# Kernel tuning notes

Measured on AMD Instinct MI355X. Metric: run time of the kernel, lower is better.

The kernel has to match this reference:

```python
import jax, jax.numpy as jnp
import numpy as np
from jax import lax

B, T = 32, 256
VOCAB, WDIM, MDIM = 50000, 300, 50
HID, NLAYERS, NCLASSES = 512, 2, 3


def _init(key, shape, scale):
    return (jax.random.normal(key, shape, dtype=jnp.float32) * scale)


def setup_inputs() -> dict:
    key = jax.random.key(0)
    ks = jax.random.split(key, 20)
    inputs_seq = jax.random.randint(ks[0], (B, T), 0, VOCAB, dtype=jnp.int32)
    masks = jax.random.randint(ks[1], (B, T), 0, 2, dtype=jnp.int32)
    length = jax.random.randint(ks[2], (B, 1), T // 2, T + 1, dtype=jnp.int32)
    embedding = _init(ks[3], (VOCAB, WDIM), 0.1)
    mask_embedding = _init(ks[4], (2, MDIM), 0.1)
    transition = _init(ks[5], (2, 2), 1.0)
    d_in0 = WDIM + MDIM          # 350
    d_in1 = 2 * HID              # 1024
    w_fw0 = _init(ks[6], (d_in0 + HID, 4 * HID), 0.02)
    b_fw0 = jnp.zeros((4 * HID,), jnp.float32)
    w_bw0 = _init(ks[7], (d_in0 + HID, 4 * HID), 0.02)
    b_bw0 = jnp.zeros((4 * HID,), jnp.float32)
    w_fw1 = _init(ks[8], (d_in1 + HID, 4 * HID), 0.02)
    b_fw1 = jnp.zeros((4 * HID,), jnp.float32)
    w_bw1 = _init(ks[9], (d_in1 + HID, 4 * HID), 0.02)
    b_bw1 = jnp.zeros((4 * HID,), jnp.float32)
    crf_w = _init(ks[10], (2 * HID, 2), 0.02)
    crf_b = jnp.zeros((2,), jnp.float32)
    logits_w = _init(ks[11], (2 * HID, NCLASSES), 0.02)
    logits_b = jnp.zeros((NCLASSES,), jnp.float32)
    return dict(inputs_seq=inputs_seq, masks=masks, length=length,
                embedding=embedding, mask_embedding=mask_embedding,
                transition=transition,
                w_fw0=w_fw0, b_fw0=b_fw0, w_bw0=w_bw0, b_bw0=b_bw0,
                w_fw1=w_fw1, b_fw1=b_fw1, w_bw1=w_bw1, b_bw1=b_bw1,
                crf_w=crf_w, crf_b=crf_b, logits_w=logits_w, logits_b=logits_b)


def _lstm_scan(x, length, W, b):
    """TF LSTMCell (gate order i, j, f, o; forget_bias=1.0) over time.
    Outputs are zeroed and state held past sequence_length (dynamic_rnn semantics)."""
    Bb, Tt, _ = x.shape
    H = W.shape[1] // 4
    zero = jnp.zeros((Bb, H), x.dtype)

    def step(carry, inp):
        h, c = carry
        xt, t = inp
        z = jnp.concatenate([xt, h], axis=-1) @ W + b
        i, j, f, o = jnp.split(z, 4, axis=-1)
        c_new = jax.nn.sigmoid(f + 1.0) * c + jax.nn.sigmoid(i) * jnp.tanh(j)
        h_new = jax.nn.sigmoid(o) * jnp.tanh(c_new)
        m = (t < length)[:, None]
        c = jnp.where(m, c_new, c)
        h = jnp.where(m, h_new, h)
        out = jnp.where(m, h_new, 0.0)
        return (h, c), out

    _, ys = lax.scan(step, (zero, zero), (x.transpose(1, 0, 2), jnp.arange(Tt)))
    return ys.transpose(1, 0, 2)  # [B,T,H]


def _reverse_seq(x, length):
    """tf.reverse_sequence along time: reverse first `length` steps, keep rest."""
    Tt = x.shape[1]
    t = jnp.arange(Tt)[None, :]
    L = length[:, None]
    idx = jnp.where(t < L, L - 1 - t, t)  # [B,T]
    return jnp.take_along_axis(x, idx[:, :, None], axis=1)


def _forward(inputs_seq, masks, length, embedding, mask_embedding, transition,
             lstm_params, crf_w, crf_b, logits_w, logits_b):
    length = length.reshape(-1)  # tf.squeeze
    emb = embedding[inputs_seq]          # [B,T,WDIM]
    memb = mask_embedding[masks]         # [B,T,MDIM]
    out = jnp.concatenate([emb, memb], axis=-1)
    for (wf, bf, wb, bb) in lstm_params:
        fw = _lstm_scan(out, length, wf, bf)
        bw = _reverse_seq(_lstm_scan(_reverse_seq(out, length), length, wb, bb), length)
        out = jnp.concatenate([fw, bw], axis=-1)  # [B,T,2H]

    # CRF forward probabilities over 2 tags
    e = out @ crf_w + crf_b              # [B,T,2] emission scores
    Tt = e.shape[1]
    alpha0 = e[:, 0]

    def crf_step(alpha, inp):
        et, t = inp
        new = jax.nn.logsumexp(alpha[:, :, None] + transition[None], axis=1) + et
        m = (t < length)[:, None]
        alpha = jnp.where(m, new, alpha)
        p = jnp.where(m, jax.nn.softmax(alpha, axis=-1), 0.0)
        return alpha, p

    _, probs_rest = lax.scan(crf_step, alpha0,
                             (e[:, 1:].transpose(1, 0, 2), jnp.arange(1, Tt)))
    p0 = jnp.where((length > 0)[:, None], jax.nn.softmax(alpha0, axis=-1), 0.0)
    probs = jnp.concatenate([p0[None], probs_rest], axis=0).transpose(1, 0, 2)  # [B,T,2]

    crf_out = probs[:, :, -1][:, None, :]            # [B,1,T]
    sentiment_vector = crf_out @ out                  # [B,1,2H]
    logits = jax.nn.softmax(sentiment_vector @ logits_w + logits_b, axis=-1)
    return logits  # [B,1,NCLASSES]


def reference(inputs_seq, masks, length, embedding, mask_embedding, transition,
              w_fw0, b_fw0, w_bw0, b_bw0, w_fw1, b_fw1, w_bw1, b_bw1,
              crf_w, crf_b, logits_w, logits_b):
    lstm_params = [(w_fw0, b_fw0, w_bw0, b_bw0), (w_fw1, b_fw1, w_bw1, b_bw1)]
    return _forward(inputs_seq, masks, length, embedding, mask_embedding,
                    transition, lstm_params, crf_w, crf_b, logits_w, logits_b)
```

## Files before the change

### kernel.cpp

```cpp
#include <hip/hip_runtime.h>
#include <hip/hip_bf16.h>
#include <cstdint>
#include <cstddef>

#define BB 32
#define TT 256
#define HID 512

typedef __attribute__((ext_vector_type(8))) short short8v;
typedef __attribute__((ext_vector_type(4))) float float4v;
typedef __attribute__((ext_vector_type(4))) unsigned int uint4v;

__device__ __forceinline__ float bf2f(unsigned short u) {
  return __uint_as_float(((unsigned int)u) << 16);
}
__device__ __forceinline__ unsigned short f2bf(float f) {
  unsigned int x = __float_as_uint(f);
  x += 0x7fffu + ((x >> 16) & 1u);
  return (unsigned short)(x >> 16);
}
__device__ __forceinline__ float fsig(float x) {
  return 1.f / (1.f + __expf(-x));
}
__device__ __forceinline__ float ftanh(float x) {
  return 1.f - 2.f / (__expf(2.f * x) + 1.f);
}

__device__ __forceinline__ void ldg4u_cohere_issue(uint4v& d, const unsigned short* p) {
  asm volatile("global_load_dwordx4 %0, %1, off sc0 sc1"
               : "=v"(d) : "v"(p) : "memory");
}
__device__ __forceinline__ void wait_vm0() {
  asm volatile("s_waitcnt vmcnt(0)" ::: "memory");
  __builtin_amdgcn_sched_barrier(0);
}

__global__ __launch_bounds__(256) void prep_all(
    const float* __restrict__ w_fw0, const float* __restrict__ w_bw0,
    const float* __restrict__ w_fw1, const float* __restrict__ w_bw1,
    unsigned short* __restrict__ wxt0f, unsigned short* __restrict__ wxt0b,
    unsigned short* __restrict__ wxt1f, unsigned short* __restrict__ wxt1b,
    unsigned short* __restrict__ whT0f, unsigned short* __restrict__ whT0b,
    unsigned short* __restrict__ whT1f, unsigned short* __restrict__ whT1b,
    const int* __restrict__ ids, const int* __restrict__ msk,
    const float* __restrict__ emb, const float* __restrict__ memb,
    unsigned short* __restrict__ x0b,
    float* __restrict__ zero_base)
{
  __shared__ float tile[64][65];
  int blk = blockIdx.x;
  int tid = threadIdx.x;
  if (blk < 2432) {
    const float* W; unsigned short* dst; int Kreal, Kpad, base;
    if (blk < 192)       { W = w_fw0; dst = wxt0f; Kreal = 350;  Kpad = 384;  base = 0; }
    else if (blk < 384)  { W = w_bw0; dst = wxt0b; Kreal = 350;  Kpad = 384;  base = 192; }
    else if (blk < 896)  { W = w_fw1; dst = wxt1f; Kreal = 1024; Kpad = 1024; base = 384; }
    else if (blk < 1408) { W = w_bw1; dst = wxt1b; Kreal = 1024; Kpad = 1024; base = 896; }
    else if (blk < 1664) { W = w_fw0 + (size_t)350 * 2048;  dst = whT0f; Kreal = 512; Kpad = 512; base = 1408; }
    else if (blk < 1920) { W = w_bw0 + (size_t)350 * 2048;  dst = whT0b; Kreal = 512; Kpad = 512; base = 1664; }
    else if (blk < 2176) { W = w_fw1 + (size_t)1024 * 2048; dst = whT1f; Kreal = 512; Kpad = 512; base = 1920; }
    else                 { W = w_bw1 + (size_t)1024 * 2048; dst = whT1b; Kreal = 512; Kpad = 512; base = 2176; }
    int rel = blk - base;
    int n0 = (rel & 31) * 64;
    int k0 = (rel >> 5) * 64;
#pragma unroll
    for (int i = 0; i < 4; ++i) {
      int e = tid + 256 * i;
      int r = e >> 4, c4 = (e & 15) * 4;
      float4 v = make_float4(0.f, 0.f, 0.f, 0.f);
      if (k0 + r < Kreal) v = *(const float4*)(W + (size_t)(k0 + r) * 2048 + n0 + c4);
      tile[r][c4 + 0] = v.x; tile[r][c4 + 1] = v.y;
      tile[r][c4 + 2] = v.z; tile[r][c4 + 3] = v.w;
    }
    __syncthreads();
    int nl = tid >> 2;
    int kg = (tid & 3) * 16;
    unsigned int pk[4], pk2[4];
#pragma unroll
    for (int jj = 0; jj < 4; ++jj) {
      unsigned short lo = f2bf(tile[kg + jj * 2 + 0][nl]);
      unsigned short hi = f2bf(tile[kg + jj * 2 + 1][nl]);
      pk[jj] = (unsigned int)lo | ((unsigned int)hi << 16);
    }
#pragma unroll
    for (int jj = 0; jj < 4; ++jj) {
      unsigned short lo = f2bf(tile[kg + 8 + jj * 2 + 0][nl]);
      unsigned short hi = f2bf(tile[kg + 8 + jj * 2 + 1][nl]);
      pk2[jj] = (unsigned int)lo | ((unsigned int)hi << 16);
    }
    size_t off = (size_t)(n0 + nl) * Kpad + k0 + kg;
    *(uint4*)(dst + off) = make_uint4(pk[0], pk[1], pk[2], pk[3]);
    *(uint4*)(dst + off + 8) = make_uint4(pk2[0], pk2[1], pk2[2], pk2[3]);
  } else if (blk < 3456) {
    int r = blk - 2432;
    int bt = r * 8 + (tid >> 5);
    int id = ids[bt];
    int m  = msk[bt];
    const float* er = emb  + (size_t)id * 300;
    const float* mr = memb + (size_t)m * 50;
    for (int d = tid & 31; d < 384; d += 32) {
      float v = (d < 300) ? er[d] : (d < 350 ? mr[d - 300] : 0.f);
      x0b[(size_t)bt * 384 + d] = f2bf(v);
    }
  } else {
    int r = blk - 3456;
    float4* p = (float4*)zero_base + (size_t)r * 1280 + tid;
#pragma unroll
    for (int i = 0; i < 5; ++i) p[i * 256] = make_float4(0.f, 0.f, 0.f, 0.f);
  }
}

__global__ __launch_bounds__(256) void gemm_xproj2(
    const unsigned short* __restrict__ A,
    const unsigned short* __restrict__ wxtF, const unsigned short* __restrict__ wxtB,
    const float* __restrict__ biasF, const float* __restrict__ biasB,
    unsigned short* __restrict__ xqF, unsigned short* __restrict__ xqB,
    int Kpad, int nkb)
{
  __shared__ unsigned short ws_s[128 * 64];
  __shared__ unsigned short xs_s[32 * 64];
  __shared__ float bias_s[128];
  int z = blockIdx.z;
  const unsigned short* wxt = z ? wxtB : wxtF;
  const float* bias = z ? biasB : biasF;
  unsigned short* xq = z ? xqB : xqF;
  int tid = threadIdx.x;
  int lane = tid & 63;
  int w = tid >> 6;
  int pos = blockIdx.x;
  int n0 = blockIdx.y * 128;
  if (tid < 128) bias_s[tid] = bias[n0 + tid];

  float4v acc[2][2];
#pragma unroll
  for (int i = 0; i < 2; ++i)
#pragma unroll
    for (int j = 0; j < 2; ++j) acc[i][j] = (float4v)0.f;

  int brow = tid >> 3;
  int seg = tid & 7;
  for (int kb = 0; kb < nkb; ++kb) {
    int k0 = kb * 64;
    __syncthreads();
    {
      const unsigned short* src = A + (size_t)(brow * 256 + pos) * Kpad + k0 + seg * 8;
      uint4 v = *(const uint4*)src;
      int o = (brow * 128 + seg * 16) ^ ((brow & 7) << 4);
      *(uint4*)((char*)xs_s + o) = v;
    }
#pragma unroll
    for (int i = 0; i < 4; ++i) {
      int n = i * 32 + brow;
      const unsigned short* src = wxt + (size_t)(n0 + n) * Kpad + k0 + seg * 8;
      uint4 v = *(const uint4*)src;
      int o = (n * 128 + seg * 16) ^ ((n & 7) << 4);
      *(uint4*)((char*)ws_s + o) = v;
    }
    __syncthreads();
#pragma unroll
    for (int kin = 0; kin < 64; kin += 32) {
      int kl = kin + ((lane >> 4) << 3);
      short8v afrag[2], bfrag[2];
#pragma unroll
      for (int nt = 0; nt < 2; ++nt) {
        int nl = w * 32 + nt * 16 + (lane & 15);
        int o = (nl * 128 + kl * 2) ^ ((nl & 7) << 4);
        afrag[nt] = *(const short8v*)((const char*)ws_s + o);
      }
#pragma unroll
      for (int bt = 0; bt < 2; ++bt) {
        int bl = bt * 16 + (lane & 15);
        int o = (bl * 128 + kl * 2) ^ ((bl & 7) << 4);
        bfrag[bt] = *(const short8v*)((const char*)xs_s + o);
      }
#pragma unroll
      for (int nt = 0; nt < 2; ++nt)
#pragma unroll
        for (int bt = 0; bt < 2; ++bt)
          acc[nt][bt] = __builtin_amdgcn_mfma_f32_16x16x32_bf16(
              afrag[nt], bfrag[bt], acc[nt][bt], 0, 0, 0);
    }
  }
  unsigned short* outp = xq + (size_t)pos * 65536;
#pragma unroll
  for (int nt = 0; nt < 2; ++nt) {
#pragma unroll
    for (int bt = 0; bt < 2; ++bt) {
#pragma unroll
      for (int reg = 0; reg < 4; ++reg) {
        int nl = w * 32 + nt * 16 + ((lane >> 4) << 2) + reg;
        int b = bt * 16 + (lane & 15);
        float v = acc[nt][bt][reg] + bias_s[nl];
        outp[(size_t)(n0 + nl) * 32 + b] = f2bf(v);
      }
    }
  }
}

__global__ __launch_bounds__(256) void lstm_mfma(
    const unsigned short* __restrict__ xq_fw, const unsigned short* __restrict__ xq_bw,
    const unsigned short* __restrict__ whT_fw, const unsigned short* __restrict__ whT_bw,
    const int* __restrict__ length,
    unsigned short* __restrict__ out,
    unsigned short* __restrict__ hT,
    float* __restrict__ cbuf,
    int* __restrict__ flags,
    int t0, int t1)
{
  extern __shared__ char smem[];
  float* zs = (float*)(smem + 65536);
  unsigned short* hb_st = (unsigned short*)(smem + 69632);
  unsigned short* ob_st = (unsigned short*)(smem + 70144);
  int tid = threadIdx.x;
  int wg = blockIdx.x;
  int dir = wg >> 6;
  int widx = wg & 63;
  int u0 = widx << 3;
  const unsigned short* xq = dir ? xq_bw : xq_fw;
  const unsigned short* whT = dir ? whT_bw : whT_fw;
  unsigned short* hbase = hT + (size_t)dir * 32768;
  int* dirflags = flags + dir * 2048;
  int* myflag = dirflags + widx * 32;

  {
    int r = tid >> 3;
    int q = r >> 3, d = r & 7;
    const unsigned short* src = whT + (size_t)(q * 512 + u0 + d) * 512 + (tid & 7) * 8;
    int ob = r * 1024 + (tid & 7) * 16;
    int sw = (r & 7) << 4;
#pragma unroll
    for (int i = 0; i < 8; ++i) {
      uint4 v = *(const uint4*)(src + i * 64);
      *(uint4*)(smem + ((ob + i * 128) ^ sw)) = v;
    }
  }

  int lane = tid & 63;
  int w = tid >> 6;
  int wr = w >> 1, wc = w & 1;
  int arow = wr * 16 + (lane & 15);
  int bcol = wc * 16 + (lane & 15);
  int chunk16 = (lane >> 4) << 4;
  int asw = (arow & 7) << 4;
  int bsw = (bcol & 7) << 4;
  int fu = tid >> 5;
  int fb = tid & 31;
  int ug = u0 + fu;
  int L = length[fb];
  float creg = 0.f;

  const unsigned short* xbase = xq + (size_t)ug * 32 + fb;
  float xv0, xv1, xv2, xv3;
  {
    int sl0 = dir ? (TT - 1 - t0) : t0;
    const unsigned short* xr = xbase + (size_t)sl0 * 65536;
    xv0 = bf2f(xr[0]);
    xv1 = bf2f(xr[16384]);
    xv2 = bf2f(xr[32768]);
    xv3 = bf2f(xr[49152]);
  }

  for (int t = t0; t < t1; ++t) {
    int sl = dir ? (TT - 1 - t) : t;
    const unsigned short* hTr_g = hbase + (size_t)(t & 1) * 16384;
    unsigned short* hTw_g = hbase + (size_t)((t & 1) ^ 1) * 16384;

    {
      int row = tid >> 3;
      int ob = 32768 + row * 1024 + (tid & 7) * 16;
      int sw = (row & 7) << 4;
      if (t == 0) {
        uint4v zv = (uint4v)0u;
#pragma unroll
        for (int i = 0; i < 8; ++i)
          *(uint4v*)(smem + ((ob + i * 128) ^ sw)) = zv;
      } else {
        const unsigned short* src = hTr_g + row * 512 + (tid & 7) * 8;
        uint4v r0, r1, r2, r3, r4, r5, r6, r7;
        ldg4u_cohere_issue(r0, src + 0 * 64);
        ldg4u_cohere_issue(r1, src + 1 * 64);
        ldg4u_cohere_issue(r2, src + 2 * 64);
        ldg4u_cohere_issue(r3, src + 3 * 64);
        ldg4u_cohere_issue(r4, src + 4 * 64);
        ldg4u_cohere_issue(r5, src + 5 * 64);
        ldg4u_cohere_issue(r6, src + 6 * 64);
        ldg4u_cohere_issue(r7, src + 7 * 64);
        wait_vm0();
        *(uint4v*)(smem + ((ob + 0 * 128) ^ sw)) = r0;
        *(uint4v*)(smem + ((ob + 1 * 128) ^ sw)) = r1;
        *(uint4v*)(smem + ((ob + 2 * 128) ^ sw)) = r2;
        *(uint4v*)(smem + ((ob + 3 * 128) ^ sw)) = r3;
        *(uint4v*)(smem + ((ob + 4 * 128) ^ sw)) = r4;
        *(uint4v*)(smem + ((ob + 5 * 128) ^ sw)) = r5;
        *(uint4v*)(smem + ((ob + 6 * 128) ^ sw)) = r6;
        *(uint4v*)(smem + ((ob + 7 * 128) ^ sw)) = r7;
      }
    }
    __syncthreads();

    float4v acc = (float4v)0.f;
#pragma unroll
    for (int ks = 0; ks < 16; ++ks) {
      int kb = ks * 64 + chunk16;
      short8v af = *(const short8v*)(smem + (size_t)arow * 1024 + (kb ^ asw));
      short8v bf = *(const short8v*)(smem + 32768 + (size_t)bcol * 1024 + (kb ^ bsw));
      acc = __builtin_amdgcn_mfma_f32_16x16x32_bf16(af, bf, acc, 0, 0, 0);
    }
#pragma unroll
    for (int r = 0; r < 4; ++r) {
      int row = wr * 16 + ((lane >> 4) << 2) + r;
      zs[row * 32 + bcol] = acc[r];
    }
    __syncthreads();

    {
      bool active = sl < L;
      float z0 = zs[(0 * 8 + fu) * 32 + fb] + xv0;
      float z1 = zs[(1 * 8 + fu) * 32 + fb] + xv1;
      float z2 = zs[(2 * 8 + fu) * 32 + fb] + xv2;
      float z3 = zs[(3 * 8 + fu) * 32 + fb] + xv3;
      int ho = 32768 + fb * 1024 + ((ug * 2) ^ ((fb & 7) << 4));
      float h_old = bf2f(*(const unsigned short*)(smem + ho));
      float c_old = cbuf ? ((t > 0) ? cbuf[dir * 16384 + ug * 32 + fb] : 0.f) : creg;
      float si = fsig(z0);
      float sj = ftanh(z1);
      float sf = fsig(z2 + 1.f);
      float so = fsig(z3);
      float cn = sf * c_old + si * sj;
      float hn = so * ftanh(cn);
      if (active) {
        if (cbuf) cbuf[dir * 16384 + ug * 32 + fb] = cn; else creg = cn;
      }
      hb_st[fb * 8 + fu] = f2bf(active ? hn : h_old);
      ob_st[fb * 8 + fu] = f2bf(active ? hn : 0.f);
    }
    __syncthreads();

    if (tid < 32) {
      uint4v hv = *(const uint4v*)(hb_st + tid * 8);
      asm volatile("global_store_dwordx4 %0, %1, off sc0 sc1"
                   :: "v"(hTw_g + tid * 512 + u0), "v"(hv) : "memory");
    } else if (tid >= 64 && tid < 96) {
      int b = tid - 64;
      uint4v ov = *(const uint4v*)(ob_st + b * 8);
      *(uint4v*)(out + (size_t)(b * TT + sl) * 1024 + dir * 512 + u0) = ov;
    }

    float nxv0 = 0.f, nxv1 = 0.f, nxv2 = 0.f, nxv3 = 0.f;
    if (t + 1 < t1) {
      int sl2 = dir ? (TT - 2 - t) : (t + 1);
      const unsigned short* xr = xbase + (size_t)sl2 * 65536;
      nxv0 = bf2f(xr[0]);
      nxv1 = bf2f(xr[16384]);
      nxv2 = bf2f(xr[32768]);
      nxv3 = bf2f(xr[49152]);
    }

    if (t1 - t0 > 1) {
      if (tid < 64) {
        wait_vm0();
        if (tid == 0) {
          __hip_atomic_store(myflag, t + 1, __ATOMIC_RELAXED,
                             __HIP_MEMORY_SCOPE_AGENT);
        }
        int* f = dirflags + tid * 32;
        while (__hip_atomic_load(f, __ATOMIC_RELAXED,
                                 __HIP_MEMORY_SCOPE_AGENT) < t + 1) {
          __builtin_amdgcn_s_sleep(1);
        }
      }
      __syncthreads();
    }
    xv0 = nxv0; xv1 = nxv1; xv2 = nxv2; xv3 = nxv3;
  }
}

__global__ __launch_bounds__(256) void crf_final(
    const unsigned short* __restrict__ out1,
    const float* __restrict__ crf_w, const float* __restrict__ crf_b,
    const float* __restrict__ trans,
    const int* __restrict__ length,
    const float* __restrict__ lw, const float* __restrict__ lb,
    float* __restrict__ dout)
{
  __shared__ float e[TT][2];
  __shared__ float pw[TT];
  __shared__ float sv[1024];
  __shared__ float red[256];
  int b = blockIdx.x, tid = threadIdx.x;
  int lane = tid & 63, w = tid >> 6;
  const unsigned short* ob = out1 + (size_t)b * TT * 1024;
  for (int t = w; t < TT; t += 4) {
    float a0 = 0.f, a1 = 0.f;
    for (int i = 0; i < 16; ++i) {
      int d = lane + i * 64;
      float v = bf2f(ob[(size_t)t * 1024 + d]);
      a0 += v * crf_w[d * 2];
      a1 += v * crf_w[d * 2 + 1];
    }
    for (int off = 32; off; off >>= 1) {
      a0 += __shfl_down(a0, off);
      a1 += __shfl_down(a1, off);
    }
    if (lane == 0) { e[t][0] = a0 + crf_b[0]; e[t][1] = a1 + crf_b[1]; }
  }
  __syncthreads();
  if (tid == 0) {
    int L = length[b];
    float t00 = trans[0], t01 = trans[1], t10 = trans[2], t11 = trans[3];
    float a0 = e[0][0], a1 = e[0][1];
    {
      float m = fmaxf(a0, a1);
      float e0 = __expf(a0 - m), e1 = __expf(a1 - m);
      pw[0] = (L > 0) ? (e1 / (e0 + e1)) : 0.f;
    }
    for (int t = 1; t < TT; ++t) {
      if (t < L) {
        float x0 = a0 + t00, y0 = a1 + t10;
        float m0 = fmaxf(x0, y0);
        float n0 = m0 + __logf(__expf(x0 - m0) + __expf(y0 - m0)) + e[t][0];
        float x1 = a0 + t01, y1 = a1 + t11;
        float m1 = fmaxf(x1, y1);
        float n1 = m1 + __logf(__expf(x1 - m1) + __expf(y1 - m1)) + e[t][1];
        a0 = n0; a1 = n1;
        float m = fmaxf(a0, a1);
        float e0 = __expf(a0 - m), e1 = __expf(a1 - m);
        pw[t] = e1 / (e0 + e1);
      } else {
        pw[t] = 0.f;
      }
    }
  }
  __syncthreads();
  for (int i = 0; i < 4; ++i) {
    int d = tid + i * 256;
    float s = 0.f;
    for (int t = 0; t < TT; ++t) s += pw[t] * bf2f(ob[(size_t)t * 1024 + d]);
    sv[d] = s;
  }
  __syncthreads();
  float v[3];
  for (int c = 0; c < 3; ++c) {
    float s = 0.f;
    for (int i = 0; i < 4; ++i) {
      int d = tid + i * 256;
      s += sv[d] * lw[d * 3 + c];
    }
    red[tid] = s;
    __syncthreads();
    for (int off = 128; off; off >>= 1) {
      if (tid < off) red[tid] += red[tid + off];
      __syncthreads();
    }
    if (tid == 0) v[c] = red[0] + lb[c];
    __syncthreads();
  }
  if (tid == 0) {
    float m = fmaxf(v[0], fmaxf(v[1], v[2]));
    float e0 = __expf(v[0] - m), e1 = __expf(v[1] - m), e2 = __expf(v[2] - m);
    float s = e0 + e1 + e2;
    dout[b * 3 + 0] = e0 / s;
    dout[b * 3 + 1] = e1 / s;
    dout[b * 3 + 2] = e2 / s;
  }
}

#define LSTM_LDS 70656

static void run_layer(const unsigned short* xq_fw, const unsigned short* xq_bw,
                      const unsigned short* whT_fw, const unsigned short* whT_bw,
                      const int* len, unsigned short* out, unsigned short* hT,
                      float* cbuf_, int* flags, hipStream_t stream) {
  const unsigned short* a0 = xq_fw; const unsigned short* a1 = xq_bw;
  const unsigned short* a2 = whT_fw; const unsigned short* a3 = whT_bw;
  const int* a4 = len; unsigned short* a5 = out; unsigned short* a6 = hT;
  float* a7 = nullptr; int* a8 = flags; int a9 = 0, a10 = TT;
  void* args[11] = { &a0, &a1, &a2, &a3, &a4, &a5, &a6, &a7, &a8, &a9, &a10 };
  hipError_t err = hipLaunchCooperativeKernel(
      reinterpret_cast<const void*>(lstm_mfma), dim3(128), dim3(256),
      args, LSTM_LDS, stream);
  if (err != hipSuccess) {
    for (int t = 0; t < TT; ++t) {
      lstm_mfma<<<128, 256, LSTM_LDS, stream>>>(
          xq_fw, xq_bw, whT_fw, whT_bw, len, out, hT, cbuf_, flags, t, t + 1);
    }
  }
}

extern "C" void kernel_launch(void* const* d_in, const int* in_sizes, int n_in,
                              void* d_out, int out_size, void* d_ws, size_t ws_size,
                              hipStream_t stream) {
  (void)in_sizes; (void)n_in; (void)out_size; (void)ws_size;
  const int* ids    = (const int*)d_in[0];
  const int* msk    = (const int*)d_in[1];
  const int* len    = (const int*)d_in[2];
  const float* emb  = (const float*)d_in[3];
  const float* memb = (const float*)d_in[4];
  const float* trans= (const float*)d_in[5];
  const float* w_fw0= (const float*)d_in[6];
  const float* b_fw0= (const float*)d_in[7];
  const float* w_bw0= (const float*)d_in[8];
  const float* b_bw0= (const float*)d_in[9];
  const float* w_fw1= (const float*)d_in[10];
  const float* b_fw1= (const float*)d_in[11];
  const float* w_bw1= (const float*)d_in[12];
  const float* b_bw1= (const float*)d_in[13];
  const float* crf_w= (const float*)d_in[14];
  const float* crf_b= (const float*)d_in[15];
  const float* lw   = (const float*)d_in[16];
  const float* lb   = (const float*)d_in[17];
  float* outp = (float*)d_out;

  float* ws = (float*)d_ws;
  unsigned short* x0b   = (unsigned short*)(ws);
  unsigned short* wxt0f = (unsigned short*)(ws + 1572864);
  unsigned short* wxt0b = (unsigned short*)(ws + 1966080);
  unsigned short* wxt1f = (unsigned short*)(ws + 2359296);
  unsigned short* wxt1b = (unsigned short*)(ws + 3407872);
  unsigned short* whT0f = (unsigned short*)(ws + 4456448);
  unsigned short* whT0b = (unsigned short*)(ws + 4980736);
  unsigned short* whT1f = (unsigned short*)(ws + 5505024);
  unsigned short* whT1b = (unsigned short*)(ws + 6029312);
  unsigned short* xqf   = (unsigned short*)(ws + 6553600);
  unsigned short* xqb   = (unsigned short*)(ws + 14942208);
  unsigned short* out0b = (unsigned short*)(ws + 23330816);
  unsigned short* out1b = (unsigned short*)(ws + 27525120);
  unsigned short* hT    = (unsigned short*)(ws + 31719424);
  float* cbuf_ = ws + 31752192;
  int*   flagsA = (int*)(ws + 31784960);
  int*   flagsB = (int*)(ws + 31789056);

  (void)hipFuncSetAttribute(reinterpret_cast<const void*>(lstm_mfma),
                            hipFuncAttributeMaxDynamicSharedMemorySize, LSTM_LDS);

  prep_all<<<3464, 256, 0, stream>>>(
      w_fw0, w_bw0, w_fw1, w_bw1,
      wxt0f, wxt0b, wxt1f, wxt1b,
      whT0f, whT0b, whT1f, whT1b,
      ids, msk, emb, memb, x0b, cbuf_);

  gemm_xproj2<<<dim3(256, 16, 2), 256, 0, stream>>>(
      x0b, wxt0f, wxt0b, b_fw0, b_bw0, xqf, xqb, 384, 6);

  run_layer(xqf, xqb, whT0f, whT0b, len, out0b, hT, cbuf_, flagsA, stream);

  gemm_xproj2<<<dim3(256, 16, 2), 256, 0, stream>>>(
      out0b, wxt1f, wxt1b, b_fw1, b_bw1, xqf, xqb, 1024, 16);

  run_layer(xqf, xqb, whT1f, whT1b, len, out1b, hT, cbuf_, flagsB, stream);

  crf_final<<<32, 256, 0, stream>>>(out1b, crf_w, crf_b, trans, len, lw, lb, outp);
}
```

Baseline: 2.004 ms.

## Replace per-step flag barrier with timestamped hidden-state packets in LSTM

The per-timestep cross-workgroup barrier (flag store plus spin on all 64 flags) is removed. Each workgroup now writes its hidden-state slice as 16-byte packets carrying the step number on both ends, and readers spin per packet until the stamps match. Consumers can therefore proceed as soon as the data they need arrives, with no separate barrier round trip. The cost is doubled hbuf traffic and per-packet polling, and the non-cooperative fallback now launches once with a spin loop, which can deadlock if not all blocks are co-resident.

```diff
diff --git a/kernel.cpp b/kernel.cpp
--- a/kernel.cpp
+++ b/kernel.cpp
@@ -10,6 +10,7 @@
 typedef __attribute__((ext_vector_type(8))) short short8v;
 typedef __attribute__((ext_vector_type(4))) float float4v;
 typedef __attribute__((ext_vector_type(4))) unsigned int uint4v;
+typedef __attribute__((ext_vector_type(2))) unsigned int uint2v;
 
 __device__ __forceinline__ float bf2f(unsigned short u) {
   return __uint_as_float(((unsigned int)u) << 16);
@@ -26,6 +27,10 @@
   return 1.f - 2.f / (__expf(2.f * x) + 1.f);
 }
 
+__device__ __forceinline__ void stg4u_cohere(unsigned short* p, uint4v v) {
+  asm volatile("global_store_dwordx4 %0, %1, off sc0 sc1"
+               :: "v"(p), "v"(v) : "memory");
+}
 __device__ __forceinline__ void ldg4u_cohere_issue(uint4v& d, const unsigned short* p) {
   asm volatile("global_load_dwordx4 %0, %1, off sc0 sc1"
                : "=v"(d) : "v"(p) : "memory");
@@ -45,7 +50,7 @@
     const int* __restrict__ ids, const int* __restrict__ msk,
     const float* __restrict__ emb, const float* __restrict__ memb,
     unsigned short* __restrict__ x0b,
-    float* __restrict__ zero_base)
+    unsigned short* __restrict__ hzero)
 {
   __shared__ float tile[64][65];
   int blk = blockIdx.x;
@@ -104,9 +109,11 @@
     }
   } else {
     int r = blk - 3456;
-    float4* p = (float4*)zero_base + (size_t)r * 1280 + tid;
-#pragma unroll
-    for (int i = 0; i < 5; ++i) p[i * 256] = make_float4(0.f, 0.f, 0.f, 0.f);
+    unsigned short* p = hzero + ((size_t)r * 2048 + tid) * 8;
+    uint4v z = (uint4v)0u;
+#pragma unroll
+    for (int i = 0; i < 8; ++i)
+      stg4u_cohere(p + (size_t)i * 256 * 8, z);
   }
 }
 
@@ -202,10 +209,7 @@
     const unsigned short* __restrict__ whT_fw, const unsigned short* __restrict__ whT_bw,
     const int* __restrict__ length,
     unsigned short* __restrict__ out,
-    unsigned short* __restrict__ hT,
-    float* __restrict__ cbuf,
-    int* __restrict__ flags,
-    int t0, int t1)
+    unsigned short* __restrict__ hbuf)
 {
   extern __shared__ char smem[];
   float* zs = (float*)(smem + 65536);
@@ -218,9 +222,6 @@
   int u0 = widx << 3;
   const unsigned short* xq = dir ? xq_bw : xq_fw;
   const unsigned short* whT = dir ? whT_bw : whT_fw;
-  unsigned short* hbase = hT + (size_t)dir * 32768;
-  int* dirflags = flags + dir * 2048;
-  int* myflag = dirflags + widx * 32;
 
   {
     int r = tid >> 3;
@@ -248,11 +249,13 @@
   int ug = u0 + fu;
   int L = length[fb];
   float creg = 0.f;
+  int pb = tid >> 3;
+  int pseg = tid & 7;
 
   const unsigned short* xbase = xq + (size_t)ug * 32 + fb;
   float xv0, xv1, xv2, xv3;
   {
-    int sl0 = dir ? (TT - 1 - t0) : t0;
+    int sl0 = dir ? (TT - 1) : 0;
     const unsigned short* xr = xbase + (size_t)sl0 * 65536;
     xv0 = bf2f(xr[0]);
     xv1 = bf2f(xr[16384]);
@@ -260,40 +263,46 @@
     xv3 = bf2f(xr[49152]);
   }
 
-  for (int t = t0; t < t1; ++t) {
+  for (int t = 0; t < TT; ++t) {
     int sl = dir ? (TT - 1 - t) : t;
-    const unsigned short* hTr_g = hbase + (size_t)(t & 1) * 16384;
-    unsigned short* hTw_g = hbase + (size_t)((t & 1) ^ 1) * 16384;
-
-    {
-      int row = tid >> 3;
-      int ob = 32768 + row * 1024 + (tid & 7) * 16;
-      int sw = (row & 7) << 4;
-      if (t == 0) {
-        uint4v zv = (uint4v)0u;
-#pragma unroll
-        for (int i = 0; i < 8; ++i)
-          *(uint4v*)(smem + ((ob + i * 128) ^ sw)) = zv;
-      } else {
-        const unsigned short* src = hTr_g + row * 512 + (tid & 7) * 8;
-        uint4v r0, r1, r2, r3, r4, r5, r6, r7;
-        ldg4u_cohere_issue(r0, src + 0 * 64);
-        ldg4u_cohere_issue(r1, src + 1 * 64);
-        ldg4u_cohere_issue(r2, src + 2 * 64);
-        ldg4u_cohere_issue(r3, src + 3 * 64);
-        ldg4u_cohere_issue(r4, src + 4 * 64);
-        ldg4u_cohere_issue(r5, src + 5 * 64);
-        ldg4u_cohere_issue(r6, src + 6 * 64);
-        ldg4u_cohere_issue(r7, src + 7 * 64);
+
+    if (t == 0) {
+      int ob = 32768 + pb * 1024 + pseg * 16;
+      int sw = (pb & 7) << 4;
+      uint4v zv = (uint4v)0u;
+#pragma unroll
+      for (int i = 0; i < 8; ++i)
+        *(uint4v*)(smem + ((ob + i * 128) ^ sw)) = zv;
+    } else {
+      unsigned stamp = (unsigned)t;
+      const unsigned short* cb = hbuf +
+          ((size_t)((dir << 1) + (t & 1)) * 4096 + (size_t)pb * 128 + pseg * 16) * 8;
+      uint4v c[16];
+#pragma unroll
+      for (int i = 0; i < 16; ++i) ldg4u_cohere_issue(c[i], cb + i * 8);
+      wait_vm0();
+      unsigned mask = 0xFFFFu;
+      while (true) {
+#pragma unroll
+        for (int i = 0; i < 16; ++i) {
+          if ((mask >> i) & 1u) {
+            if (c[i].x == stamp && c[i].w == stamp) {
+              int kb = pseg * 16 + i;
+              int off = (32768 + pb * 1024 + kb * 8) ^ ((pb & 7) << 4);
+              uint2v d2;
+              d2.x = c[i].y;
+              d2.y = c[i].z;
+              *(uint2v*)(smem + off) = d2;
+              mask &= ~(1u << i);
+            }
+          }
+        }
+        if (!mask) break;
+        __builtin_amdgcn_s_sleep(1);
+#pragma unroll
+        for (int i = 0; i < 16; ++i)
+          if ((mask >> i) & 1u) ldg4u_cohere_issue(c[i], cb + i * 8);
         wait_vm0();
-        *(uint4v*)(smem + ((ob + 0 * 128) ^ sw)) = r0;
-        *(uint4v*)(smem + ((ob + 1 * 128) ^ sw)) = r1;
-        *(uint4v*)(smem + ((ob + 2 * 128) ^ sw)) = r2;
-        *(uint4v*)(smem + ((ob + 3 * 128) ^ sw)) = r3;
-        *(uint4v*)(smem + ((ob + 4 * 128) ^ sw)) = r4;
-        *(uint4v*)(smem + ((ob + 5 * 128) ^ sw)) = r5;
-        *(uint4v*)(smem + ((ob + 6 * 128) ^ sw)) = r6;
-        *(uint4v*)(smem + ((ob + 7 * 128) ^ sw)) = r7;
       }
     }
     __syncthreads();
@@ -321,57 +330,44 @@
       float z3 = zs[(3 * 8 + fu) * 32 + fb] + xv3;
       int ho = 32768 + fb * 1024 + ((ug * 2) ^ ((fb & 7) << 4));
       float h_old = bf2f(*(const unsigned short*)(smem + ho));
-      float c_old = cbuf ? ((t > 0) ? cbuf[dir * 16384 + ug * 32 + fb] : 0.f) : creg;
       float si = fsig(z0);
       float sj = ftanh(z1);
       float sf = fsig(z2 + 1.f);
       float so = fsig(z3);
-      float cn = sf * c_old + si * sj;
+      float cn = sf * creg + si * sj;
       float hn = so * ftanh(cn);
-      if (active) {
-        if (cbuf) cbuf[dir * 16384 + ug * 32 + fb] = cn; else creg = cn;
-      }
+      if (active) creg = cn;
       hb_st[fb * 8 + fu] = f2bf(active ? hn : h_old);
       ob_st[fb * 8 + fu] = f2bf(active ? hn : 0.f);
     }
     __syncthreads();
 
-    if (tid < 32) {
-      uint4v hv = *(const uint4v*)(hb_st + tid * 8);
-      asm volatile("global_store_dwordx4 %0, %1, off sc0 sc1"
-                   :: "v"(hTw_g + tid * 512 + u0), "v"(hv) : "memory");
+    if (tid < 64) {
+      int b = tid >> 1, j = tid & 1;
+      uint2v d = *(const uint2v*)(hb_st + b * 8 + j * 4);
+      uint4v ch;
+      ch.x = (unsigned)(t + 1);
+      ch.y = d.x;
+      ch.z = d.y;
+      ch.w = (unsigned)(t + 1);
+      unsigned short* dst = hbuf +
+          ((size_t)((dir << 1) + ((t + 1) & 1)) * 4096 + (size_t)b * 128 +
+           (2 * widx + j)) * 8;
+      stg4u_cohere(dst, ch);
     } else if (tid >= 64 && tid < 96) {
       int b = tid - 64;
       uint4v ov = *(const uint4v*)(ob_st + b * 8);
       *(uint4v*)(out + (size_t)(b * TT + sl) * 1024 + dir * 512 + u0) = ov;
     }
 
-    float nxv0 = 0.f, nxv1 = 0.f, nxv2 = 0.f, nxv3 = 0.f;
-    if (t + 1 < t1) {
+    if (t + 1 < TT) {
       int sl2 = dir ? (TT - 2 - t) : (t + 1);
       const unsigned short* xr = xbase + (size_t)sl2 * 65536;
-      nxv0 = bf2f(xr[0]);
-      nxv1 = bf2f(xr[16384]);
-      nxv2 = bf2f(xr[32768]);
-      nxv3 = bf2f(xr[49152]);
-    }
-
-    if (t1 - t0 > 1) {
-      if (tid < 64) {
-        wait_vm0();
-        if (tid == 0) {
-          __hip_atomic_store(myflag, t + 1, __ATOMIC_RELAXED,
-                             __HIP_MEMORY_SCOPE_AGENT);
-        }
-        int* f = dirflags + tid * 32;
-        while (__hip_atomic_load(f, __ATOMIC_RELAXED,
-                                 __HIP_MEMORY_SCOPE_AGENT) < t + 1) {
-          __builtin_amdgcn_s_sleep(1);
-        }
-      }
-      __syncthreads();
-    }
-    xv0 = nxv0; xv1 = nxv1; xv2 = nxv2; xv3 = nxv3;
+      xv0 = bf2f(xr[0]);
+      xv1 = bf2f(xr[16384]);
+      xv2 = bf2f(xr[32768]);
+      xv3 = bf2f(xr[49152]);
+    }
   }
 }
 
@@ -469,21 +465,18 @@
 
 static void run_layer(const unsigned short* xq_fw, const unsigned short* xq_bw,
                       const unsigned short* whT_fw, const unsigned short* whT_bw,
-                      const int* len, unsigned short* out, unsigned short* hT,
-                      float* cbuf_, int* flags, hipStream_t stream) {
+                      const int* len, unsigned short* out, unsigned short* hbuf,
+                      hipStream_t stream) {
   const unsigned short* a0 = xq_fw; const unsigned short* a1 = xq_bw;
   const unsigned short* a2 = whT_fw; const unsigned short* a3 = whT_bw;
-  const int* a4 = len; unsigned short* a5 = out; unsigned short* a6 = hT;
-  float* a7 = nullptr; int* a8 = flags; int a9 = 0, a10 = TT;
-  void* args[11] = { &a0, &a1, &a2, &a3, &a4, &a5, &a6, &a7, &a8, &a9, &a10 };
+  const int* a4 = len; unsigned short* a5 = out; unsigned short* a6 = hbuf;
+  void* args[7] = { &a0, &a1, &a2, &a3, &a4, &a5, &a6 };
   hipError_t err = hipLaunchCooperativeKernel(
       reinterpret_cast<const void*>(lstm_mfma), dim3(128), dim3(256),
       args, LSTM_LDS, stream);
   if (err != hipSuccess) {
-    for (int t = 0; t < TT; ++t) {
-      lstm_mfma<<<128, 256, LSTM_LDS, stream>>>(
-          xq_fw, xq_bw, whT_fw, whT_bw, len, out, hT, cbuf_, flags, t, t + 1);
-    }
+    lstm_mfma<<<128, 256, LSTM_LDS, stream>>>(
+        xq_fw, xq_bw, whT_fw, whT_bw, len, out, hbuf);
   }
 }
 
@@ -525,29 +518,27 @@
   unsigned short* xqb   = (unsigned short*)(ws + 14942208);
   unsigned short* out0b = (unsigned short*)(ws + 23330816);
   unsigned short* out1b = (unsigned short*)(ws + 27525120);
-  unsigned short* hT    = (unsigned short*)(ws + 31719424);
-  float* cbuf_ = ws + 31752192;
-  int*   flagsA = (int*)(ws + 31784960);
-  int*   flagsB = (int*)(ws + 31789056);
+  unsigned short* hbufA = (unsigned short*)(ws + 31719424);
+  unsigned short* hbufB = (unsigned short*)(ws + 31784960);
 
   (void)hipFuncSetAttribute(reinterpret_cast<const void*>(lstm_mfma),
                             hipFuncAttributeMaxDynamicSharedMemorySize, LSTM_LDS);
 
-  prep_all<<<3464, 256, 0, stream>>>(
+  prep_all<<<3472, 256, 0, stream>>>(
       w_fw0, w_bw0, w_fw1, w_bw1,
       wxt0f, wxt0b, wxt1f, wxt1b,
       whT0f, whT0b, whT1f, whT1b,
-      ids, msk, emb, memb, x0b, cbuf_);
+      ids, msk, emb, memb, x0b, hbufA);
 
   gemm_xproj2<<<dim3(256, 16, 2), 256, 0, stream>>>(
       x0b, wxt0f, wxt0b, b_fw0, b_bw0, xqf, xqb, 384, 6);
 
-  run_layer(xqf, xqb, whT0f, whT0b, len, out0b, hT, cbuf_, flagsA, stream);
+  run_layer(xqf, xqb, whT0f, whT0b, len, out0b, hbufA, stream);
 
   gemm_xproj2<<<dim3(256, 16, 2), 256, 0, stream>>>(
       out0b, wxt1f, wxt1b, b_fw1, b_bw1, xqf, xqb, 1024, 16);
 
-  run_layer(xqf, xqb, whT1f, whT1b, len, out1b, hT, cbuf_, flagsB, stream);
+  run_layer(xqf, xqb, whT1f, whT1b, len, out1b, hbufB, stream);
 
   crf_final<<<32, 256, 0, stream>>>(out1b, crf_w, crf_b, trans, len, lw, lb, outp);
 }
```

Result: slower. 3.703 ms (+84.8%).
